# Performance work log

Hardware: AMD Instinct MI355X
Metric: run time of the kernel (lower is better)

Reference implementation:

```python
import jax, jax.numpy as jnp
import numpy as np

B, F = 512, 512
K, D = 32, 16  # num_kernels, dim_per_kernel


def setup_inputs() -> dict:
    key = jax.random.key(0)
    kx, kt = jax.random.split(key)
    x = jax.random.normal(kx, (B, F), dtype=jnp.float32)
    # keras 'uniform' init is small-range uniform; scale similarly
    T = jax.random.uniform(kt, (F, K * D), dtype=jnp.float32, minval=-0.05, maxval=0.05)
    return {"x": x, "T": T}


def reference(x, T):
    # m: [B, K, D]
    m = (x @ T).reshape(-1, K, D)
    # all-pairs L1 distance per kernel: [B, B, K]
    abs_diffs = jnp.sum(jnp.abs(m[:, None, :, :] - m[None, :, :, :]), axis=-1)
    # minibatch features: sum_j exp(-||m_i - m_j||_1) -> [B, K]
    feats = jnp.sum(jnp.exp(-abs_diffs), axis=1)
    return jnp.concatenate([x, feats], axis=1)
```

## Files before the change

### kernel.cpp

```cpp
#include <hip/hip_runtime.h>
#include <hip/hip_bf16.h>
#include <math.h>

#define BSZ 512
#define FDIM 512
#define NK 32
#define DD 16
#define NDIM (NK*DD)
#define OUTW (FDIM + NK)

typedef __attribute__((ext_vector_type(8))) short short8;
typedef __attribute__((ext_vector_type(4))) float float4v;

static __device__ __forceinline__ short f2bf(float f) {
  return (short)__builtin_bit_cast(unsigned short, __float2bfloat16(f));
}

__global__ __launch_bounds__(256) void k_gemm(
    const float* __restrict__ x, const float* __restrict__ T,
    float* __restrict__ m, float* __restrict__ out) {
  const int t  = threadIdx.x;
  const int b  = blockIdx.x;
  const int rg = b >> 5, cg = b & 31;
  const int r0 = rg * 16, c0 = cg * 16;
  const int lane = t & 63;
  const int w    = __builtin_amdgcn_readfirstlane(t >> 6);
  const int mi   = lane & 15;
  const int q    = lane >> 4;

  const float* __restrict__ xa = x + (size_t)(r0 + mi) * FDIM + 128 * w + 8 * q;
  const float* __restrict__ tb = T + (size_t)(128 * w + 8 * q) * NDIM + c0 + mi;

  float4v acc = {0.f, 0.f, 0.f, 0.f};
#pragma unroll
  for (int j = 0; j < 4; ++j) {
    const float4 a0 = *(const float4*)(xa + 32 * j);
    const float4 a1 = *(const float4*)(xa + 32 * j + 4);
    float bv[8];
#pragma unroll
    for (int i = 0; i < 8; ++i) bv[i] = tb[(size_t)(32 * j + i) * NDIM];
    short8 af, bf;
    af[0] = f2bf(a0.x); af[1] = f2bf(a0.y); af[2] = f2bf(a0.z); af[3] = f2bf(a0.w);
    af[4] = f2bf(a1.x); af[5] = f2bf(a1.y); af[6] = f2bf(a1.z); af[7] = f2bf(a1.w);
#pragma unroll
    for (int i = 0; i < 8; ++i) bf[i] = f2bf(bv[i]);
    acc = __builtin_amdgcn_mfma_f32_16x16x32_bf16(af, bf, acc, 0, 0, 0);
  }

  __shared__ float red[4][16][16];
#pragma unroll
  for (int r = 0; r < 4; ++r) red[w][q * 4 + r][mi] = acc[r];
  __syncthreads();
  {
    const int orow = t >> 4, ocol = t & 15;
    const float s = red[0][orow][ocol] + red[1][orow][ocol] +
                    red[2][orow][ocol] + red[3][orow][ocol];
    m[(size_t)(r0 + orow) * NDIM + c0 + ocol] = s;
  }

  const int g = b * 256 + t;
  if (g < 65536) {
    const int orow = g >> 7, c4 = g & 127;
    *(float4*)(out + (size_t)orow * OUTW + c4 * 4) =
        *(const float4*)(x + (size_t)orow * FDIM + c4 * 4);
  } else if (g < 65536 + 16384) {
    const int idx = g - 65536;
    const int orow = idx >> 5, kk = idx & 31;
    out[(size_t)orow * OUTW + FDIM + kk] = 0.f;
  }
}

__global__ __launch_bounds__(256) void k_dist(
    const float* __restrict__ m, float* __restrict__ out) {
  __shared__ float Bs[128 * DD];
  __shared__ float red[256];
  const int t   = threadIdx.x;
  const int bid = blockIdx.x;
  const int ig  = bid >> 7;
  const int k   = (bid >> 2) & 31;
  const int jq  = bid & 3;
  const int lane = t & 63;
  const int i    = ig * 64 + lane;

  const float4* ap = (const float4*)(m + (size_t)i * NDIM + k * DD);
  const float4 A0 = ap[0], A1 = ap[1], A2 = ap[2], A3 = ap[3];

  const float* mb = m + (size_t)(jq * 128) * NDIM + k * DD;
#pragma unroll
  for (int qq = 0; qq < 2; ++qq) {
    const int idx = qq * 256 + t;
    const int jrow = idx >> 2, part = idx & 3;
    *(float4*)&Bs[jrow * DD + part * 4] =
        *(const float4*)(mb + (size_t)jrow * NDIM + part * 4);
  }
  __syncthreads();

  float a[DD];
  a[0]=A0.x; a[1]=A0.y; a[2]=A0.z;  a[3]=A0.w;
  a[4]=A1.x; a[5]=A1.y; a[6]=A1.z;  a[7]=A1.w;
  a[8]=A2.x; a[9]=A2.y; a[10]=A2.z; a[11]=A2.w;
  a[12]=A3.x;a[13]=A3.y;a[14]=A3.z; a[15]=A3.w;

  const int w = __builtin_amdgcn_readfirstlane(t >> 6);
  const int jbase = w * 32;
  float f = 0.f;
#pragma unroll 4
  for (int j = 0; j < 32; ++j) {
    const float4* bp = (const float4*)&Bs[(jbase + j) * DD];
    const float4 b0 = bp[0], b1 = bp[1], b2 = bp[2], b3 = bp[3];
    float d =
        fabsf(a[0]  - b0.x) + fabsf(a[1]  - b0.y) +
        fabsf(a[2]  - b0.z) + fabsf(a[3]  - b0.w) +
        fabsf(a[4]  - b1.x) + fabsf(a[5]  - b1.y) +
        fabsf(a[6]  - b1.z) + fabsf(a[7]  - b1.w) +
        fabsf(a[8]  - b2.x) + fabsf(a[9]  - b2.y) +
        fabsf(a[10] - b2.z) + fabsf(a[11] - b2.w) +
        fabsf(a[12] - b3.x) + fabsf(a[13] - b3.y) +
        fabsf(a[14] - b3.z) + fabsf(a[15] - b3.w);
    f += __expf(-d);
  }

  red[t] = f;
  __syncthreads();
  if (t < 64) {
    const float s = red[t] + red[t + 64] + red[t + 128] + red[t + 192];
    atomicAdd(out + (size_t)(ig * 64 + t) * OUTW + FDIM + k, s);
  }
}

extern "C" void kernel_launch(void* const* d_in, const int* in_sizes, int n_in,
                              void* d_out, int out_size, void* d_ws,
                              size_t ws_size, hipStream_t stream) {
  (void)in_sizes; (void)n_in; (void)out_size; (void)ws_size;
  const float* x = (const float*)d_in[0];
  const float* T = (const float*)d_in[1];
  float* out = (float*)d_out;
  float* m   = (float*)d_ws;

  hipLaunchKernelGGL(k_gemm, dim3(1024), dim3(256), 0, stream, x, T, m, out);
  hipLaunchKernelGGL(k_dist, dim3(1024), dim3(256), 0, stream, m, out);
}
```

Before: 72.36 us.

## Add prep kernel converting x and transposed T to bf16 before GEMM

```diff
diff --git a/kernel.cpp b/kernel.cpp
--- a/kernel.cpp
+++ b/kernel.cpp
@@ -12,13 +12,60 @@
 typedef __attribute__((ext_vector_type(8))) short short8;
 typedef __attribute__((ext_vector_type(4))) float float4v;
 
-static __device__ __forceinline__ short f2bf(float f) {
-  return (short)__builtin_bit_cast(unsigned short, __float2bfloat16(f));
+static __device__ __forceinline__ unsigned short f2bfu(float f) {
+  return __builtin_bit_cast(unsigned short, __float2bfloat16(f));
 }
 
-__global__ __launch_bounds__(256) void k_gemm(
+__global__ __launch_bounds__(256) void k_prep(
     const float* __restrict__ x, const float* __restrict__ T,
-    float* __restrict__ m, float* __restrict__ out) {
+    unsigned short* __restrict__ xbf, unsigned short* __restrict__ tbf,
+    float* __restrict__ out) {
+  const int t = threadIdx.x, b = blockIdx.x;
+  if (b < 64) {
+    __shared__ unsigned short lt[64][65];
+    const int tr = b >> 3, tc = b & 7;
+    const float4* T4 = (const float4*)T;
+#pragma unroll
+    for (int qi = 0; qi < 4; ++qi) {
+      const int idx = qi * 256 + t;
+      const int rr = idx >> 4, c4 = idx & 15;
+      const float4 v = T4[(size_t)(tr * 64 + rr) * 128 + tc * 16 + c4];
+      lt[c4 * 4 + 0][rr] = f2bfu(v.x);
+      lt[c4 * 4 + 1][rr] = f2bfu(v.y);
+      lt[c4 * 4 + 2][rr] = f2bfu(v.z);
+      lt[c4 * 4 + 3][rr] = f2bfu(v.w);
+    }
+    __syncthreads();
+#pragma unroll
+    for (int qi = 0; qi < 8; ++qi) {
+      const int idx = qi * 256 + t;
+      const int cl = idx >> 5, sg = idx & 31;
+      ushort2 p;
+      p.x = lt[cl][sg * 2];
+      p.y = lt[cl][sg * 2 + 1];
+      *(ushort2*)(tbf + (size_t)(tc * 64 + cl) * 512 + tr * 64 + sg * 2) = p;
+    }
+  } else {
+    const int bb = b - 64;
+    const float4* x4 = (const float4*)x;
+#pragma unroll
+    for (int qi = 0; qi < 4; ++qi) {
+      const int i = bb * 1024 + qi * 256 + t;
+      const float4 v = x4[i];
+      const int orow = i >> 7, c4 = i & 127;
+      *(float4*)(out + (size_t)orow * OUTW + c4 * 4) = v;
+      ushort4 u;
+      u.x = f2bfu(v.x); u.y = f2bfu(v.y); u.z = f2bfu(v.z); u.w = f2bfu(v.w);
+      *(ushort4*)(xbf + (size_t)i * 4) = u;
+    }
+    const int idx2 = bb * 256 + t;
+    out[(size_t)(idx2 >> 5) * OUTW + FDIM + (idx2 & 31)] = 0.f;
+  }
+}
+
+__global__ __launch_bounds__(256, 4) void k_gemm(
+    const unsigned short* __restrict__ xbf,
+    const unsigned short* __restrict__ tbf, float* __restrict__ m) {
   const int t  = threadIdx.x;
   const int b  = blockIdx.x;
   const int rg = b >> 5, cg = b & 31;
@@ -28,24 +75,21 @@
   const int mi   = lane & 15;
   const int q    = lane >> 4;
 
-  const float* __restrict__ xa = x + (size_t)(r0 + mi) * FDIM + 128 * w + 8 * q;
-  const float* __restrict__ tb = T + (size_t)(128 * w + 8 * q) * NDIM + c0 + mi;
+  const unsigned short* __restrict__ xa =
+      xbf + (size_t)(r0 + mi) * FDIM + 128 * w + 8 * q;
+  const unsigned short* __restrict__ tb =
+      tbf + (size_t)(c0 + mi) * FDIM + 128 * w + 8 * q;
 
+  short8 af[4], bf[4];
+#pragma unroll
+  for (int j = 0; j < 4; ++j) {
+    af[j] = *(const short8*)(xa + 32 * j);
+    bf[j] = *(const short8*)(tb + 32 * j);
+  }
   float4v acc = {0.f, 0.f, 0.f, 0.f};
 #pragma unroll
-  for (int j = 0; j < 4; ++j) {
-    const float4 a0 = *(const float4*)(xa + 32 * j);
-    const float4 a1 = *(const float4*)(xa + 32 * j + 4);
-    float bv[8];
-#pragma unroll
-    for (int i = 0; i < 8; ++i) bv[i] = tb[(size_t)(32 * j + i) * NDIM];
-    short8 af, bf;
-    af[0] = f2bf(a0.x); af[1] = f2bf(a0.y); af[2] = f2bf(a0.z); af[3] = f2bf(a0.w);
-    af[4] = f2bf(a1.x); af[5] = f2bf(a1.y); af[6] = f2bf(a1.z); af[7] = f2bf(a1.w);
-#pragma unroll
-    for (int i = 0; i < 8; ++i) bf[i] = f2bf(bv[i]);
-    acc = __builtin_amdgcn_mfma_f32_16x16x32_bf16(af, bf, acc, 0, 0, 0);
-  }
+  for (int j = 0; j < 4; ++j)
+    acc = __builtin_amdgcn_mfma_f32_16x16x32_bf16(af[j], bf[j], acc, 0, 0, 0);
 
   __shared__ float red[4][16][16];
 #pragma unroll
@@ -56,17 +100,6 @@
     const float s = red[0][orow][ocol] + red[1][orow][ocol] +
                     red[2][orow][ocol] + red[3][orow][ocol];
     m[(size_t)(r0 + orow) * NDIM + c0 + ocol] = s;
-  }
-
-  const int g = b * 256 + t;
-  if (g < 65536) {
-    const int orow = g >> 7, c4 = g & 127;
-    *(float4*)(out + (size_t)orow * OUTW + c4 * 4) =
-        *(const float4*)(x + (size_t)orow * FDIM + c4 * 4);
-  } else if (g < 65536 + 16384) {
-    const int idx = g - 65536;
-    const int orow = idx >> 5, kk = idx & 31;
-    out[(size_t)orow * OUTW + FDIM + kk] = 0.f;
   }
 }
 
@@ -135,8 +168,12 @@
   const float* x = (const float*)d_in[0];
   const float* T = (const float*)d_in[1];
   float* out = (float*)d_out;
-  float* m   = (float*)d_ws;
+  float* m = (float*)d_ws;
+  unsigned short* xbf = (unsigned short*)((char*)d_ws + (size_t)BSZ * NDIM * 4);
+  unsigned short* tbf = xbf + (size_t)BSZ * FDIM;
 
-  hipLaunchKernelGGL(k_gemm, dim3(1024), dim3(256), 0, stream, x, T, m, out);
+  hipLaunchKernelGGL(k_prep, dim3(128), dim3(256), 0, stream,
+                     x, T, xbf, tbf, out);
+  hipLaunchKernelGGL(k_gemm, dim3(1024), dim3(256), 0, stream, xbf, tbf, m);
   hipLaunchKernelGGL(k_dist, dim3(1024), dim3(256), 0, stream, m, out);
 }
```

New measurement: 74.25 us. +2.6%, slower.
